# Performance work log

Measured on AMD Instinct MI355X. Metric: run time of the kernel, lower is better.

## Reference

```python
import jax, jax.numpy as jnp
import numpy as np

B, L, D, T = 64, 1500, 768, 240000  # batch, emb_time, feature_dim, raw_time (T = 160*L)

def setup_inputs() -> dict:
    key = jax.random.key(0)
    k1, k2, k3, k4 = jax.random.split(key, 4)
    embeddings = jax.random.normal(k1, (B, L, D), dtype=jnp.float32)
    # per-sample valid lengths in [T//2, T]; pad_mask True == padded position
    lengths = jax.random.randint(k2, (B,), T // 2, T + 1)
    pad_mask = jnp.arange(T)[None, :] >= lengths[:, None]  # (B, T) bool
    W1 = jax.random.normal(k3, (2 * D, D), dtype=jnp.float32) * (1.0 / np.sqrt(D))
    W2 = jax.random.normal(k4, (D, 2 * D), dtype=jnp.float32) * (1.0 / np.sqrt(2 * D))
    return {"embeddings": embeddings, "W1": W1, "W2": W2, "pad_mask": pad_mask}

def reference(embeddings, W1, W2, pad_mask):
    # embeddings: (B, L, D); pad_mask: (B, T) with T = 160*L, True for padded.
    Braw, Lemb, Dm = embeddings.shape
    Traw = pad_mask.shape[1]
    # F.adaptive_avg_pool1d(pad_mask.float(), L) with T divisible by L == bin-mean
    pooled = pad_mask.astype(jnp.float32).reshape(Braw, Lemb, Traw // Lemb).mean(axis=-1)
    # downsampled_mask = pooled > 0 (any padding in bin); unpadded = ~that
    valid = (pooled <= 0).astype(embeddings.dtype)  # (B, L), 1 where bin fully unpadded
    cnt = valid.sum(axis=1, keepdims=True)          # (B, 1), >0 by construction
    # fused masked mean (replaces the per-sample python loop)
    mean_emb = jnp.einsum('bld,bl->bd', embeddings, valid) / cnt  # (B, D)
    # neck: Linear(D->2D, no bias), ReLU, Linear(2D->D, no bias)
    h = jax.nn.relu(mean_emb @ W1.T)
    out = h @ W2.T
    # F.normalize(dim=-1, p=2)
    return out / jnp.linalg.norm(out, axis=-1, keepdims=True)
```

## Files before the change

kernel.cpp:

```cpp
#include <hip/hip_runtime.h>

#define BB 64
#define LL 1500
#define DD 768
#define TT 240000
#define BIN 160
#define NCH 30
#define LCH 50
#define TWO_D 1536
#define NJ1 8
#define ND2 4

#define OFF_PARTIAL 0
#define OFF_LEN     5898240
#define OFF_MEANT   5898496
#define OFF_HT      6095104
#define OFF_RAW     6488320

__global__ __launch_bounds__(192) void k_partial(const float* __restrict__ emb,
                                                 const unsigned int* __restrict__ mask,
                                                 float* __restrict__ partial,
                                                 int* __restrict__ lenb) {
    int w = blockIdx.x;
    int b = w / NCH, c = w % NCH, t = threadIdx.x;
    int lane = t & 63;

    int lo = TT / 2, hi = TT;
    while (hi > lo) {
        int step = (hi - lo + 63) / 64;
        int p = lo + lane * step;
        unsigned int v = (p >= hi) ? 1u : mask[(size_t)b * TT + p];
        unsigned long long bal = __ballot(v != 0u);
        int f = __ffsll((unsigned long long)bal) - 1;
        if (f < 0) {
            lo = lo + 63 * step + 1;
            if (lo > hi) lo = hi;
        } else {
            int new_hi = lo + f * step;
            int new_lo = (f == 0) ? lo : (lo + (f - 1) * step + 1);
            lo = new_lo;
            hi = (new_hi < hi) ? new_hi : hi;
        }
    }
    int len = lo;
    if (c == 0 && t == 0) lenb[b] = len;

    int fl = len / BIN;
    int n = fl - c * LCH;
    n = (n < 0) ? 0 : ((n > LCH) ? LCH : n);

    float* pout = partial + (size_t)w * DD + 4 * t;
    if (n == 0) {
        float4 z = {0.f, 0.f, 0.f, 0.f};
        *(float4*)pout = z;
        return;
    }

    const float* ebase = emb + ((size_t)b * LL + c * LCH) * DD + 4 * t;
    float4 acc = {0.f, 0.f, 0.f, 0.f};
    if (n == LCH) {
        for (int i0 = 0; i0 < LCH; i0 += 10) {
#pragma unroll
            for (int j = 0; j < 10; ++j) {
                float4 v = *(const float4*)(ebase + (size_t)(i0 + j) * DD);
                acc.x += v.x; acc.y += v.y; acc.z += v.z; acc.w += v.w;
            }
        }
    } else {
        int nr = ((n + 4) / 5) * 5;
        for (int i0 = 0; i0 < nr; i0 += 5) {
#pragma unroll
            for (int j = 0; j < 5; ++j) {
                int i = i0 + j;
                float4 v = *(const float4*)(ebase + (size_t)i * DD);
                float f = (i < n) ? 1.0f : 0.0f;
                acc.x = fmaf(f, v.x, acc.x);
                acc.y = fmaf(f, v.y, acc.y);
                acc.z = fmaf(f, v.z, acc.z);
                acc.w = fmaf(f, v.w, acc.w);
            }
        }
    }
    *(float4*)pout = acc;
}

__global__ void k_meanT(const float* __restrict__ partial,
                        const int* __restrict__ lenb,
                        float* __restrict__ meanT) {
    int bid = blockIdx.x;
    int b = bid / 3, slab = bid % 3;
    int q = slab * 64 + threadIdx.x;
    float cnt = (float)(lenb[b] / BIN);
    const float4* pb = (const float4*)(partial + (size_t)b * NCH * DD) + q;
    float4 s = {0.f, 0.f, 0.f, 0.f};
#pragma unroll 10
    for (int c = 0; c < NCH; ++c) {
        float4 v = pb[(size_t)c * (DD / 4)];
        s.x += v.x; s.y += v.y; s.z += v.z; s.w += v.w;
    }
    float inv = 1.0f / cnt;
    int d = 4 * q;
    meanT[(size_t)(d + 0) * BB + b] = s.x * inv;
    meanT[(size_t)(d + 1) * BB + b] = s.y * inv;
    meanT[(size_t)(d + 2) * BB + b] = s.z * inv;
    meanT[(size_t)(d + 3) * BB + b] = s.w * inv;
}

__global__ __launch_bounds__(256) void k_fc1T(const float* __restrict__ meanT,
                                              const float* __restrict__ W1,
                                              float* __restrict__ hT) {
    int j0 = blockIdx.x * NJ1;
    int wid = threadIdx.x >> 6, lane = threadIdx.x & 63;
    const float* mp    = meanT + (size_t)(wid * (DD / 4)) * BB + lane;
    const float* wbase = W1 + (size_t)j0 * DD + wid * (DD / 4);
    float acc[NJ1] = {0.f, 0.f, 0.f, 0.f, 0.f, 0.f, 0.f, 0.f};
    for (int k = 0; k < DD / 4; k += 8) {
        float m0 = mp[(size_t)(k + 0) * BB];
        float m1 = mp[(size_t)(k + 1) * BB];
        float m2 = mp[(size_t)(k + 2) * BB];
        float m3 = mp[(size_t)(k + 3) * BB];
        float m4 = mp[(size_t)(k + 4) * BB];
        float m5 = mp[(size_t)(k + 5) * BB];
        float m6 = mp[(size_t)(k + 6) * BB];
        float m7 = mp[(size_t)(k + 7) * BB];
#pragma unroll
        for (int jj = 0; jj < NJ1; ++jj) {
            const float* wr = wbase + (size_t)jj * DD + k;
            float4 wa = *(const float4*)(wr);
            float4 wb = *(const float4*)(wr + 4);
            float a = acc[jj];
            a = fmaf(wa.x, m0, a); a = fmaf(wa.y, m1, a);
            a = fmaf(wa.z, m2, a); a = fmaf(wa.w, m3, a);
            a = fmaf(wb.x, m4, a); a = fmaf(wb.y, m5, a);
            a = fmaf(wb.z, m6, a); a = fmaf(wb.w, m7, a);
            acc[jj] = a;
        }
    }
    __shared__ float sh[4][NJ1][BB];
#pragma unroll
    for (int jj = 0; jj < NJ1; ++jj) sh[wid][jj][lane] = acc[jj];
    __syncthreads();
    for (int idx = threadIdx.x; idx < NJ1 * BB; idx += 256) {
        int jj = idx >> 6, b2 = idx & 63;
        float r = (sh[0][jj][b2] + sh[1][jj][b2]) + (sh[2][jj][b2] + sh[3][jj][b2]);
        hT[(size_t)(j0 + jj) * BB + b2] = fmaxf(r, 0.0f);
    }
}

__global__ __launch_bounds__(256) void k_fc2T(const float* __restrict__ hT,
                                              const float* __restrict__ W2,
                                              float* __restrict__ raw) {
    int d0 = blockIdx.x * ND2;
    int wid = threadIdx.x >> 6, lane = threadIdx.x & 63;
    const float* hp    = hT + (size_t)(wid * (TWO_D / 4)) * BB + lane;
    const float* wbase = W2 + (size_t)d0 * TWO_D + wid * (TWO_D / 4);
    float acc[ND2] = {0.f, 0.f, 0.f, 0.f};
    for (int k = 0; k < TWO_D / 4; k += 8) {
        float h0 = hp[(size_t)(k + 0) * BB];
        float h1 = hp[(size_t)(k + 1) * BB];
        float h2 = hp[(size_t)(k + 2) * BB];
        float h3 = hp[(size_t)(k + 3) * BB];
        float h4 = hp[(size_t)(k + 4) * BB];
        float h5 = hp[(size_t)(k + 5) * BB];
        float h6 = hp[(size_t)(k + 6) * BB];
        float h7 = hp[(size_t)(k + 7) * BB];
#pragma unroll
        for (int dd = 0; dd < ND2; ++dd) {
            const float* wr = wbase + (size_t)dd * TWO_D + k;
            float4 wa = *(const float4*)(wr);
            float4 wb = *(const float4*)(wr + 4);
            float a = acc[dd];
            a = fmaf(wa.x, h0, a); a = fmaf(wa.y, h1, a);
            a = fmaf(wa.z, h2, a); a = fmaf(wa.w, h3, a);
            a = fmaf(wb.x, h4, a); a = fmaf(wb.y, h5, a);
            a = fmaf(wb.z, h6, a); a = fmaf(wb.w, h7, a);
            acc[dd] = a;
        }
    }
    __shared__ float sh[4][ND2][BB];
#pragma unroll
    for (int dd = 0; dd < ND2; ++dd) sh[wid][dd][lane] = acc[dd];
    __syncthreads();
    {
        int idx = threadIdx.x;
        int dd = idx >> 6, b2 = idx & 63;
        float r = (sh[0][dd][b2] + sh[1][dd][b2]) + (sh[2][dd][b2] + sh[3][dd][b2]);
        raw[(size_t)b2 * DD + d0 + dd] = r;
    }
}

__global__ void k_norm(const float* __restrict__ raw, float* __restrict__ out) {
    int b = blockIdx.x, t = threadIdx.x;
    float v0 = raw[b * DD + t];
    float v1 = raw[b * DD + 256 + t];
    float v2 = raw[b * DD + 512 + t];
    float s = v0 * v0 + v1 * v1 + v2 * v2;
    for (int off = 32; off; off >>= 1) s += __shfl_down(s, off);
    __shared__ float sh[4];
    __shared__ float inv_s;
    int wave = t >> 6, lane = t & 63;
    if (lane == 0) sh[wave] = s;
    __syncthreads();
    if (t == 0) inv_s = 1.0f / sqrtf(sh[0] + sh[1] + sh[2] + sh[3]);
    __syncthreads();
    float inv = inv_s;
    out[b * DD + t]       = v0 * inv;
    out[b * DD + 256 + t] = v1 * inv;
    out[b * DD + 512 + t] = v2 * inv;
}

extern "C" void kernel_launch(void* const* d_in, const int* in_sizes, int n_in,
                              void* d_out, int out_size, void* d_ws, size_t ws_size,
                              hipStream_t stream) {
    const float* emb         = (const float*)d_in[0];
    const float* W1          = (const float*)d_in[1];
    const float* W2          = (const float*)d_in[2];
    const unsigned int* mask = (const unsigned int*)d_in[3];

    char* ws = (char*)d_ws;
    float* partial = (float*)(ws + OFF_PARTIAL);
    int*   lenb    = (int*)(ws + OFF_LEN);
    float* meanT   = (float*)(ws + OFF_MEANT);
    float* hT      = (float*)(ws + OFF_HT);
    float* raw     = (float*)(ws + OFF_RAW);
    float* out     = (float*)d_out;

    k_partial<<<BB * NCH, 192, 0, stream>>>(emb, mask, partial, lenb);
    k_meanT<<<192, 64, 0, stream>>>(partial, lenb, meanT);
    k_fc1T<<<TWO_D / NJ1, 256, 0, stream>>>(meanT, W1, hT);
    k_fc2T<<<DD / ND2, 256, 0, stream>>>(hT, W2, raw);
    k_norm<<<BB, 256, 0, stream>>>(raw, out);
}
```

Before: 78.11 us.

## Fuse mean, FC1, FC2 and normalize into one cooperative kernel with grid syncs

Replaces the four small tail kernels (mean reduction, FC1, FC2, L2 normalize) with a single cooperative launch of 192 blocks. Stages are separated by grid-wide barriers instead of separate kernel launches. The aim is to remove launch gaps and per-kernel ramp-up between tiny dependent stages. The cost is three grid.sync barriers and the overhead of a cooperative launch.

```diff
diff --git a/kernel.cpp b/kernel.cpp
--- a/kernel.cpp
+++ b/kernel.cpp
@@ -1,4 +1,7 @@
 #include <hip/hip_runtime.h>
+#include <hip/hip_cooperative_groups.h>
+
+namespace cg = cooperative_groups;
 
 #define BB 64
 #define LL 1500
@@ -84,129 +87,138 @@
     *(float4*)pout = acc;
 }
 
-__global__ void k_meanT(const float* __restrict__ partial,
-                        const int* __restrict__ lenb,
-                        float* __restrict__ meanT) {
-    int bid = blockIdx.x;
-    int b = bid / 3, slab = bid % 3;
-    int q = slab * 64 + threadIdx.x;
-    float cnt = (float)(lenb[b] / BIN);
-    const float4* pb = (const float4*)(partial + (size_t)b * NCH * DD) + q;
-    float4 s = {0.f, 0.f, 0.f, 0.f};
+__global__ __launch_bounds__(256) void k_tail(const float* __restrict__ partial,
+                                              const int* __restrict__ lenb,
+                                              const float* __restrict__ W1,
+                                              const float* __restrict__ W2,
+                                              float* __restrict__ meanT,
+                                              float* __restrict__ hT,
+                                              float* __restrict__ raw,
+                                              float* __restrict__ out) {
+    cg::grid_group grid = cg::this_grid();
+    __shared__ float shbuf[4 * NJ1 * BB];
+    int wid = threadIdx.x >> 6, lane = threadIdx.x & 63;
+
+    {
+        int idx = blockIdx.x * 256 + threadIdx.x;
+        if (idx < BB * (DD / 4)) {
+            int b = idx / (DD / 4), q = idx % (DD / 4);
+            float cnt = (float)(lenb[b] / BIN);
+            const float4* pb = (const float4*)(partial + (size_t)b * NCH * DD) + q;
+            float4 s = {0.f, 0.f, 0.f, 0.f};
 #pragma unroll 10
-    for (int c = 0; c < NCH; ++c) {
-        float4 v = pb[(size_t)c * (DD / 4)];
-        s.x += v.x; s.y += v.y; s.z += v.z; s.w += v.w;
-    }
-    float inv = 1.0f / cnt;
-    int d = 4 * q;
-    meanT[(size_t)(d + 0) * BB + b] = s.x * inv;
-    meanT[(size_t)(d + 1) * BB + b] = s.y * inv;
-    meanT[(size_t)(d + 2) * BB + b] = s.z * inv;
-    meanT[(size_t)(d + 3) * BB + b] = s.w * inv;
-}
-
-__global__ __launch_bounds__(256) void k_fc1T(const float* __restrict__ meanT,
-                                              const float* __restrict__ W1,
-                                              float* __restrict__ hT) {
-    int j0 = blockIdx.x * NJ1;
-    int wid = threadIdx.x >> 6, lane = threadIdx.x & 63;
-    const float* mp    = meanT + (size_t)(wid * (DD / 4)) * BB + lane;
-    const float* wbase = W1 + (size_t)j0 * DD + wid * (DD / 4);
-    float acc[NJ1] = {0.f, 0.f, 0.f, 0.f, 0.f, 0.f, 0.f, 0.f};
-    for (int k = 0; k < DD / 4; k += 8) {
-        float m0 = mp[(size_t)(k + 0) * BB];
-        float m1 = mp[(size_t)(k + 1) * BB];
-        float m2 = mp[(size_t)(k + 2) * BB];
-        float m3 = mp[(size_t)(k + 3) * BB];
-        float m4 = mp[(size_t)(k + 4) * BB];
-        float m5 = mp[(size_t)(k + 5) * BB];
-        float m6 = mp[(size_t)(k + 6) * BB];
-        float m7 = mp[(size_t)(k + 7) * BB];
-#pragma unroll
-        for (int jj = 0; jj < NJ1; ++jj) {
-            const float* wr = wbase + (size_t)jj * DD + k;
-            float4 wa = *(const float4*)(wr);
-            float4 wb = *(const float4*)(wr + 4);
-            float a = acc[jj];
-            a = fmaf(wa.x, m0, a); a = fmaf(wa.y, m1, a);
-            a = fmaf(wa.z, m2, a); a = fmaf(wa.w, m3, a);
-            a = fmaf(wb.x, m4, a); a = fmaf(wb.y, m5, a);
-            a = fmaf(wb.z, m6, a); a = fmaf(wb.w, m7, a);
-            acc[jj] = a;
-        }
-    }
-    __shared__ float sh[4][NJ1][BB];
-#pragma unroll
-    for (int jj = 0; jj < NJ1; ++jj) sh[wid][jj][lane] = acc[jj];
-    __syncthreads();
-    for (int idx = threadIdx.x; idx < NJ1 * BB; idx += 256) {
-        int jj = idx >> 6, b2 = idx & 63;
-        float r = (sh[0][jj][b2] + sh[1][jj][b2]) + (sh[2][jj][b2] + sh[3][jj][b2]);
-        hT[(size_t)(j0 + jj) * BB + b2] = fmaxf(r, 0.0f);
-    }
-}
-
-__global__ __launch_bounds__(256) void k_fc2T(const float* __restrict__ hT,
-                                              const float* __restrict__ W2,
-                                              float* __restrict__ raw) {
-    int d0 = blockIdx.x * ND2;
-    int wid = threadIdx.x >> 6, lane = threadIdx.x & 63;
-    const float* hp    = hT + (size_t)(wid * (TWO_D / 4)) * BB + lane;
-    const float* wbase = W2 + (size_t)d0 * TWO_D + wid * (TWO_D / 4);
-    float acc[ND2] = {0.f, 0.f, 0.f, 0.f};
-    for (int k = 0; k < TWO_D / 4; k += 8) {
-        float h0 = hp[(size_t)(k + 0) * BB];
-        float h1 = hp[(size_t)(k + 1) * BB];
-        float h2 = hp[(size_t)(k + 2) * BB];
-        float h3 = hp[(size_t)(k + 3) * BB];
-        float h4 = hp[(size_t)(k + 4) * BB];
-        float h5 = hp[(size_t)(k + 5) * BB];
-        float h6 = hp[(size_t)(k + 6) * BB];
-        float h7 = hp[(size_t)(k + 7) * BB];
-#pragma unroll
-        for (int dd = 0; dd < ND2; ++dd) {
-            const float* wr = wbase + (size_t)dd * TWO_D + k;
-            float4 wa = *(const float4*)(wr);
-            float4 wb = *(const float4*)(wr + 4);
-            float a = acc[dd];
-            a = fmaf(wa.x, h0, a); a = fmaf(wa.y, h1, a);
-            a = fmaf(wa.z, h2, a); a = fmaf(wa.w, h3, a);
-            a = fmaf(wb.x, h4, a); a = fmaf(wb.y, h5, a);
-            a = fmaf(wb.z, h6, a); a = fmaf(wb.w, h7, a);
-            acc[dd] = a;
-        }
-    }
-    __shared__ float sh[4][ND2][BB];
-#pragma unroll
-    for (int dd = 0; dd < ND2; ++dd) sh[wid][dd][lane] = acc[dd];
-    __syncthreads();
+            for (int c = 0; c < NCH; ++c) {
+                float4 v = pb[(size_t)c * (DD / 4)];
+                s.x += v.x; s.y += v.y; s.z += v.z; s.w += v.w;
+            }
+            float inv = 1.0f / cnt;
+            int d = 4 * q;
+            meanT[(size_t)(d + 0) * BB + b] = s.x * inv;
+            meanT[(size_t)(d + 1) * BB + b] = s.y * inv;
+            meanT[(size_t)(d + 2) * BB + b] = s.z * inv;
+            meanT[(size_t)(d + 3) * BB + b] = s.w * inv;
+        }
+    }
+    grid.sync();
+
     {
-        int idx = threadIdx.x;
-        int dd = idx >> 6, b2 = idx & 63;
-        float r = (sh[0][dd][b2] + sh[1][dd][b2]) + (sh[2][dd][b2] + sh[3][dd][b2]);
-        raw[(size_t)b2 * DD + d0 + dd] = r;
-    }
-}
-
-__global__ void k_norm(const float* __restrict__ raw, float* __restrict__ out) {
-    int b = blockIdx.x, t = threadIdx.x;
-    float v0 = raw[b * DD + t];
-    float v1 = raw[b * DD + 256 + t];
-    float v2 = raw[b * DD + 512 + t];
-    float s = v0 * v0 + v1 * v1 + v2 * v2;
-    for (int off = 32; off; off >>= 1) s += __shfl_down(s, off);
-    __shared__ float sh[4];
-    __shared__ float inv_s;
-    int wave = t >> 6, lane = t & 63;
-    if (lane == 0) sh[wave] = s;
-    __syncthreads();
-    if (t == 0) inv_s = 1.0f / sqrtf(sh[0] + sh[1] + sh[2] + sh[3]);
-    __syncthreads();
-    float inv = inv_s;
-    out[b * DD + t]       = v0 * inv;
-    out[b * DD + 256 + t] = v1 * inv;
-    out[b * DD + 512 + t] = v2 * inv;
+        int j0 = blockIdx.x * NJ1;
+        const float* mp    = meanT + (size_t)(wid * (DD / 4)) * BB + lane;
+        const float* wbase = W1 + (size_t)j0 * DD + wid * (DD / 4);
+        float acc[NJ1] = {0.f, 0.f, 0.f, 0.f, 0.f, 0.f, 0.f, 0.f};
+        for (int k = 0; k < DD / 4; k += 8) {
+            float m0 = mp[(size_t)(k + 0) * BB];
+            float m1 = mp[(size_t)(k + 1) * BB];
+            float m2 = mp[(size_t)(k + 2) * BB];
+            float m3 = mp[(size_t)(k + 3) * BB];
+            float m4 = mp[(size_t)(k + 4) * BB];
+            float m5 = mp[(size_t)(k + 5) * BB];
+            float m6 = mp[(size_t)(k + 6) * BB];
+            float m7 = mp[(size_t)(k + 7) * BB];
+#pragma unroll
+            for (int jj = 0; jj < NJ1; ++jj) {
+                const float* wr = wbase + (size_t)jj * DD + k;
+                float4 wa = *(const float4*)(wr);
+                float4 wb = *(const float4*)(wr + 4);
+                float a = acc[jj];
+                a = fmaf(wa.x, m0, a); a = fmaf(wa.y, m1, a);
+                a = fmaf(wa.z, m2, a); a = fmaf(wa.w, m3, a);
+                a = fmaf(wb.x, m4, a); a = fmaf(wb.y, m5, a);
+                a = fmaf(wb.z, m6, a); a = fmaf(wb.w, m7, a);
+                acc[jj] = a;
+            }
+        }
+        float (*sh)[NJ1][BB] = (float (*)[NJ1][BB])shbuf;
+#pragma unroll
+        for (int jj = 0; jj < NJ1; ++jj) sh[wid][jj][lane] = acc[jj];
+        __syncthreads();
+        for (int idx = threadIdx.x; idx < NJ1 * BB; idx += 256) {
+            int jj = idx >> 6, b2 = idx & 63;
+            float r = (sh[0][jj][b2] + sh[1][jj][b2]) + (sh[2][jj][b2] + sh[3][jj][b2]);
+            hT[(size_t)(j0 + jj) * BB + b2] = fmaxf(r, 0.0f);
+        }
+    }
+    grid.sync();
+
+    {
+        int d0 = blockIdx.x * ND2;
+        const float* hp    = hT + (size_t)(wid * (TWO_D / 4)) * BB + lane;
+        const float* wbase = W2 + (size_t)d0 * TWO_D + wid * (TWO_D / 4);
+        float acc[ND2] = {0.f, 0.f, 0.f, 0.f};
+        for (int k = 0; k < TWO_D / 4; k += 8) {
+            float h0 = hp[(size_t)(k + 0) * BB];
+            float h1 = hp[(size_t)(k + 1) * BB];
+            float h2 = hp[(size_t)(k + 2) * BB];
+            float h3 = hp[(size_t)(k + 3) * BB];
+            float h4 = hp[(size_t)(k + 4) * BB];
+            float h5 = hp[(size_t)(k + 5) * BB];
+            float h6 = hp[(size_t)(k + 6) * BB];
+            float h7 = hp[(size_t)(k + 7) * BB];
+#pragma unroll
+            for (int dd = 0; dd < ND2; ++dd) {
+                const float* wr = wbase + (size_t)dd * TWO_D + k;
+                float4 wa = *(const float4*)(wr);
+                float4 wb = *(const float4*)(wr + 4);
+                float a = acc[dd];
+                a = fmaf(wa.x, h0, a); a = fmaf(wa.y, h1, a);
+                a = fmaf(wa.z, h2, a); a = fmaf(wa.w, h3, a);
+                a = fmaf(wb.x, h4, a); a = fmaf(wb.y, h5, a);
+                a = fmaf(wb.z, h6, a); a = fmaf(wb.w, h7, a);
+                acc[dd] = a;
+            }
+        }
+        float (*sh)[ND2][BB] = (float (*)[ND2][BB])shbuf;
+        __syncthreads();
+#pragma unroll
+        for (int dd = 0; dd < ND2; ++dd) sh[wid][dd][lane] = acc[dd];
+        __syncthreads();
+        {
+            int idx = threadIdx.x;
+            int dd = idx >> 6, b2 = idx & 63;
+            float r = (sh[0][dd][b2] + sh[1][dd][b2]) + (sh[2][dd][b2] + sh[3][dd][b2]);
+            raw[(size_t)b2 * DD + d0 + dd] = r;
+        }
+    }
+    grid.sync();
+
+    if (blockIdx.x < BB) {
+        int b = blockIdx.x, t = threadIdx.x;
+        float v0 = raw[b * DD + t];
+        float v1 = raw[b * DD + 256 + t];
+        float v2 = raw[b * DD + 512 + t];
+        float s = v0 * v0 + v1 * v1 + v2 * v2;
+        for (int off = 32; off; off >>= 1) s += __shfl_down(s, off);
+        float* sh = shbuf;
+        __syncthreads();
+        if ((t & 63) == 0) sh[t >> 6] = s;
+        __syncthreads();
+        if (t == 0) sh[4] = 1.0f / sqrtf(sh[0] + sh[1] + sh[2] + sh[3]);
+        __syncthreads();
+        float inv = sh[4];
+        out[b * DD + t]       = v0 * inv;
+        out[b * DD + 256 + t] = v1 * inv;
+        out[b * DD + 512 + t] = v2 * inv;
+    }
 }
 
 extern "C" void kernel_launch(void* const* d_in, const int* in_sizes, int n_in,
@@ -226,8 +238,8 @@
     float* out     = (float*)d_out;
 
     k_partial<<<BB * NCH, 192, 0, stream>>>(emb, mask, partial, lenb);
-    k_meanT<<<192, 64, 0, stream>>>(partial, lenb, meanT);
-    k_fc1T<<<TWO_D / NJ1, 256, 0, stream>>>(meanT, W1, hT);
-    k_fc2T<<<DD / ND2, 256, 0, stream>>>(hT, W2, raw);
-    k_norm<<<BB, 256, 0, stream>>>(raw, out);
+
+    void* args[] = {&partial, &lenb, &W1, &W2, &meanT, &hT, &raw, &out};
+    hipLaunchCooperativeKernel((void*)k_tail, dim3(192), dim3(256),
+                               args, 0, stream);
 }
```

Measured after the change: 151.9 us. +94.5%, slower.
